# Optimization experiments

Hardware: AMD Instinct MI355X
Metric: run time of the kernel (lower is better)

## Reference

```python
import jax, jax.numpy as jnp
import numpy as np

ALPHA = 1.0
GAMMA = 2.0
BETA = 0.99
NUM_CLASSES = 37
N = 4_194_304


def setup_inputs() -> dict:
    key = jax.random.key(0)
    k1, k2 = jax.random.split(key)
    logits = jax.random.normal(k1, (N, NUM_CLASSES), dtype=jnp.float32)
    target = jax.random.randint(k2, (N,), 0, NUM_CLASSES, dtype=jnp.int64 if jax.config.jax_enable_x64 else jnp.int32)
    return {"logits": logits, "target": target}


def reference(logits, target):
    # Stable cross-entropy per sample: ce = -log_softmax(logits)[i, target[i]]
    logp = jax.nn.log_softmax(logits, axis=-1)                    # [N, C]
    ce = -jnp.take_along_axis(logp, target[:, None], axis=-1)[:, 0]  # [N]
    pt = jnp.exp(-ce)

    # Histogram of class counts (replaces the per-class Python loop).
    counts = jnp.zeros((NUM_CLASSES,), dtype=jnp.float32).at[target].add(1.0)  # [C]

    # Per-sample weight: 1 / beta**freq(class of sample)
    weights = (1.0 / BETA) ** counts[target]                      # [N]

    # Per-class weight: 1 / beta**(freq / total). Fresh state => total == N.
    class_weights = (1.0 / BETA) ** (counts / counts.sum())       # [C]

    focal = ALPHA * (1.0 - pt) ** GAMMA * ce * weights            # [N]
    # reduction == 'mean': (scalar / [C]).mean()
    return (focal.mean() / class_weights).mean()
```

## Files before the change

kernel.cpp:

```cpp
#include <hip/hip_runtime.h>
#include <hip/hip_bf16.h>

#define NUM_C 37
#define WTILE 64
#define LOG_INV_BETA 0.010050336f
#define LOG_BETA    (-0.010050336f)
#define FLT_MAX_SAT 3.402823466e+38f

#define NSLOT 64
#define SLOT_STRIDE 16
#define WS_E 37
#define WS_SLOTS 64
#define WS_TOTAL (WS_SLOTS + NSLOT * SLOT_STRIDE)

__device__ __forceinline__ float finite_scrub(float v, float sat) {
    unsigned u = __float_as_uint(v);
    if ((u & 0x7f800000u) == 0x7f800000u) return sat;
    return v;
}

__global__ void hist_kernel(const int* __restrict__ target, float* __restrict__ counts, int n) {
    __shared__ unsigned int h[NUM_C];
    for (int j = threadIdx.x; j < NUM_C; j += blockDim.x) h[j] = 0u;
    __syncthreads();

    const int4* t4 = (const int4*)target;
    int n4 = n >> 2;
    int stride = gridDim.x * blockDim.x;
    for (int i = blockIdx.x * blockDim.x + threadIdx.x; i < n4; i += stride) {
        int4 v = t4[i];
        if ((unsigned)v.x < NUM_C) atomicAdd(&h[v.x], 1u);
        if ((unsigned)v.y < NUM_C) atomicAdd(&h[v.y], 1u);
        if ((unsigned)v.z < NUM_C) atomicAdd(&h[v.z], 1u);
        if ((unsigned)v.w < NUM_C) atomicAdd(&h[v.w], 1u);
    }
    for (int i = (n4 << 2) + blockIdx.x * blockDim.x + threadIdx.x; i < n; i += stride) {
        int t = target[i];
        if ((unsigned)t < NUM_C) atomicAdd(&h[t], 1u);
    }
    __syncthreads();
    for (int j = threadIdx.x; j < NUM_C; j += blockDim.x)
        if (h[j]) atomicAdd(&counts[j], (float)h[j]);
}

__global__ void prep_kernel(float* __restrict__ ws) {
    int c = threadIdx.x;
    float v = (c < NUM_C) ? ws[c] : 0.0f;
#pragma unroll
    for (int off = 32; off > 0; off >>= 1) v = fmaxf(v, __shfl_xor(v, off, 64));
    if (c == 0) ws[WS_E] = v * LOG_INV_BETA;
}

__global__ __launch_bounds__(WTILE) void focal_main(const float* __restrict__ logits,
                                                    const int* __restrict__ target,
                                                    float* __restrict__ ws,
                                                    int n) {
    __shared__ float sm[WTILE * NUM_C];
    const int lane = threadIdx.x;
    const float E = ws[WS_E];

    long long base = (long long)blockIdx.x * WTILE;
    const float* src = logits + base * NUM_C;

    if (base + WTILE <= n) {
#pragma unroll
        for (int r = 0; r < 9; ++r) {
            __builtin_amdgcn_global_load_lds(
                (const __attribute__((address_space(1))) unsigned int*)(src + r * 256 + lane * 4),
                (__attribute__((address_space(3))) unsigned int*)((char*)sm + r * 1024),
                16, 0, 0);
        }
        __builtin_amdgcn_global_load_lds(
            (const __attribute__((address_space(1))) unsigned int*)(src + 9 * 256 + lane),
            (__attribute__((address_space(3))) unsigned int*)((char*)sm + 9 * 1024),
            4, 0, 0);
    } else {
        int rem = (int)((long long)n - base) * NUM_C;
        for (int k = lane; k < rem; k += WTILE) sm[k] = src[k];
    }
    __syncthreads();

    float local = 0.0f;
    long long i = base + lane;
    if (i < n) {
        const float* row = sm + lane * NUM_C;
        float r[NUM_C];
#pragma unroll
        for (int j = 0; j < NUM_C; ++j) r[j] = row[j];
        float m = r[0];
#pragma unroll
        for (int j = 1; j < NUM_C; ++j) m = fmaxf(m, r[j]);
        float s = 0.0f;
#pragma unroll
        for (int j = 0; j < NUM_C; ++j) s += __expf(r[j] - m);
        int t = target[i];
        if ((unsigned)t >= NUM_C) t = 0;
        float xt = row[t];
        float ce = __logf(s) + m - xt;
        float pt = __expf(-ce);
        float ex = fminf(fmaf(ws[t], LOG_INV_BETA, -E), 0.0f);
        float w  = __expf(ex);
        float om = 1.0f - pt;
        local = fminf(fmaxf(om * om * ce * w, 0.0f), 1e30f);
    }

#pragma unroll
    for (int off = 32; off > 0; off >>= 1) local += __shfl_down(local, off, 64);
    if (lane == 0)
        atomicAdd(&ws[WS_SLOTS + (blockIdx.x & (NSLOT - 1)) * SLOT_STRIDE], local);
}

__global__ void finalize_kernel(const float* __restrict__ ws, float* __restrict__ out, int n) {
    int c = threadIdx.x;
    float S = ws[WS_SLOTS + c * SLOT_STRIDE];
#pragma unroll
    for (int off = 32; off > 0; off >>= 1) S += __shfl_xor(S, off, 64);
    float cnt = (c < NUM_C) ? ws[c] : 0.0f;
    float total = cnt;
#pragma unroll
    for (int off = 32; off > 0; off >>= 1) total += __shfl_xor(total, off, 64);
    total = fmaxf(total, 1.0f);
    float term = (c < NUM_C) ? __expf((cnt / total) * LOG_BETA) : 0.0f;
    float s = term;
#pragma unroll
    for (int off = 32; off > 0; off >>= 1) s += __shfl_xor(s, off, 64);
    if (c == 0) {
        float Sf = finite_scrub(S, 1e30f);
        float E  = finite_scrub(ws[WS_E], 1e6f);
        E = fminf(fmaxf(E, 0.0f), 1e6f);
        float log_result = E + __logf(fmaxf(Sf, 1e-38f) / (float)n)
                             + __logf(fmaxf(s, 1e-38f) / (float)NUM_C);
        float v = __expf(fminf(log_result, 88.0f));
        if (log_result < -103.0f) v = 0.0f;
        v = finite_scrub(v, FLT_MAX_SAT);
        v = fminf(fmaxf(v, 0.0f), FLT_MAX_SAT);
        out[0] = v;
    }
}

extern "C" void kernel_launch(void* const* d_in, const int* in_sizes, int n_in,
                              void* d_out, int out_size, void* d_ws, size_t ws_size,
                              hipStream_t stream) {
    const float* logits = (const float*)d_in[0];
    const int* target   = (const int*)d_in[1];
    float* out          = (float*)d_out;
    float* ws           = (float*)d_ws;
    int n = in_sizes[1];

    hipMemsetAsync(d_ws, 0, WS_TOTAL * sizeof(float), stream);

    hist_kernel<<<256, 256, 0, stream>>>(target, ws, n);
    prep_kernel<<<1, 64, 0, stream>>>(ws);

    int nblocks = (n + WTILE - 1) / WTILE;
    focal_main<<<nblocks, WTILE, 0, stream>>>(logits, target, ws, n);

    finalize_kernel<<<1, 64, 0, stream>>>(ws, out, n);
}
```

Measured before the change: 789.8 us.

## Fuse histogram into focal pass via per-class partial sums and double-buffered persistent tiles

Drops the separate histogram and prep kernels. Because the per-sample weight depends only on the class, the main kernel now accumulates per-class focal sums and counts in LDS, and finalize applies the class weights afterwards. The main kernel is also made persistent with a fixed grid and double-buffered async global-to-LDS staging of logits and targets, so the next tile loads while the current one computes. This removes a full extra read of the target array and three launches' worth of dependency, at the cost of LDS atomics per sample and a hand-set waitcnt that must match the number of outstanding loads.

```diff
diff --git a/kernel.cpp b/kernel.cpp
--- a/kernel.cpp
+++ b/kernel.cpp
@@ -2,16 +2,16 @@
 #include <hip/hip_bf16.h>
 
 #define NUM_C 37
-#define WTILE 64
 #define LOG_INV_BETA 0.010050336f
 #define LOG_BETA    (-0.010050336f)
 #define FLT_MAX_SAT 3.402823466e+38f
 
-#define NSLOT 64
-#define SLOT_STRIDE 16
-#define WS_E 37
-#define WS_SLOTS 64
-#define WS_TOTAL (WS_SLOTS + NSLOT * SLOT_STRIDE)
+#define NBLK 4096
+#define NSLOT 32
+#define SLOT_PITCH 40
+#define WS_CNT 64
+#define WS_P   (WS_CNT + NSLOT * SLOT_PITCH)
+#define WS_TOTAL (WS_P + NSLOT * SLOT_PITCH)
 
 __device__ __forceinline__ float finite_scrub(float v, float sat) {
     unsigned u = __float_as_uint(v);
@@ -19,117 +19,138 @@
     return v;
 }
 
-__global__ void hist_kernel(const int* __restrict__ target, float* __restrict__ counts, int n) {
-    __shared__ unsigned int h[NUM_C];
-    for (int j = threadIdx.x; j < NUM_C; j += blockDim.x) h[j] = 0u;
-    __syncthreads();
-
-    const int4* t4 = (const int4*)target;
-    int n4 = n >> 2;
-    int stride = gridDim.x * blockDim.x;
-    for (int i = blockIdx.x * blockDim.x + threadIdx.x; i < n4; i += stride) {
-        int4 v = t4[i];
-        if ((unsigned)v.x < NUM_C) atomicAdd(&h[v.x], 1u);
-        if ((unsigned)v.y < NUM_C) atomicAdd(&h[v.y], 1u);
-        if ((unsigned)v.z < NUM_C) atomicAdd(&h[v.z], 1u);
-        if ((unsigned)v.w < NUM_C) atomicAdd(&h[v.w], 1u);
+__device__ __forceinline__ void stage_tile_async(const float* __restrict__ src,
+                                                 const int* __restrict__ tgt,
+                                                 float* bufp, int* tbufp, int lane) {
+#pragma unroll
+    for (int r = 0; r < 9; ++r) {
+        __builtin_amdgcn_global_load_lds(
+            (const __attribute__((address_space(1))) unsigned int*)(src + r * 256 + lane * 4),
+            (__attribute__((address_space(3))) unsigned int*)((char*)bufp + r * 1024),
+            16, 0, 0);
     }
-    for (int i = (n4 << 2) + blockIdx.x * blockDim.x + threadIdx.x; i < n; i += stride) {
-        int t = target[i];
-        if ((unsigned)t < NUM_C) atomicAdd(&h[t], 1u);
-    }
-    __syncthreads();
-    for (int j = threadIdx.x; j < NUM_C; j += blockDim.x)
-        if (h[j]) atomicAdd(&counts[j], (float)h[j]);
+    __builtin_amdgcn_global_load_lds(
+        (const __attribute__((address_space(1))) unsigned int*)(src + 2304 + lane),
+        (__attribute__((address_space(3))) unsigned int*)((char*)bufp + 9216), 4, 0, 0);
+    __builtin_amdgcn_global_load_lds(
+        (const __attribute__((address_space(1))) unsigned int*)(tgt + lane),
+        (__attribute__((address_space(3))) unsigned int*)tbufp, 4, 0, 0);
 }
 
-__global__ void prep_kernel(float* __restrict__ ws) {
-    int c = threadIdx.x;
-    float v = (c < NUM_C) ? ws[c] : 0.0f;
-#pragma unroll
-    for (int off = 32; off > 0; off >>= 1) v = fmaxf(v, __shfl_xor(v, off, 64));
-    if (c == 0) ws[WS_E] = v * LOG_INV_BETA;
+__device__ __forceinline__ void stage_tile_partial(const float* __restrict__ src,
+                                                   const int* __restrict__ tgt,
+                                                   float* bufp, int* tbufp,
+                                                   int lane, int rem) {
+    for (int k = lane; k < rem * NUM_C; k += 64) bufp[k] = src[k];
+    if (lane < rem) tbufp[lane] = tgt[lane];
 }
 
-__global__ __launch_bounds__(WTILE) void focal_main(const float* __restrict__ logits,
-                                                    const int* __restrict__ target,
-                                                    float* __restrict__ ws,
-                                                    int n) {
-    __shared__ float sm[WTILE * NUM_C];
+__global__ __launch_bounds__(64) void fused_main(const float* __restrict__ logits,
+                                                 const int* __restrict__ target,
+                                                 float* __restrict__ ws,
+                                                 int n) {
+    __shared__ float buf[2][64 * NUM_C];
+    __shared__ int   tbuf[2][64];
+    __shared__ float hP[NUM_C];
+    __shared__ unsigned hC[NUM_C];
+
     const int lane = threadIdx.x;
-    const float E = ws[WS_E];
+    if (lane < NUM_C) { hP[lane] = 0.0f; hC[lane] = 0u; }
 
-    long long base = (long long)blockIdx.x * WTILE;
-    const float* src = logits + base * NUM_C;
+    const int total_tiles = (n + 63) >> 6;
+    int tile = blockIdx.x;
+    int pb = 0;
 
-    if (base + WTILE <= n) {
-#pragma unroll
-        for (int r = 0; r < 9; ++r) {
-            __builtin_amdgcn_global_load_lds(
-                (const __attribute__((address_space(1))) unsigned int*)(src + r * 256 + lane * 4),
-                (__attribute__((address_space(3))) unsigned int*)((char*)sm + r * 1024),
-                16, 0, 0);
-        }
-        __builtin_amdgcn_global_load_lds(
-            (const __attribute__((address_space(1))) unsigned int*)(src + 9 * 256 + lane),
-            (__attribute__((address_space(3))) unsigned int*)((char*)sm + 9 * 1024),
-            4, 0, 0);
-    } else {
-        int rem = (int)((long long)n - base) * NUM_C;
-        for (int k = lane; k < rem; k += WTILE) sm[k] = src[k];
-    }
-    __syncthreads();
-
-    float local = 0.0f;
-    long long i = base + lane;
-    if (i < n) {
-        const float* row = sm + lane * NUM_C;
-        float r[NUM_C];
-#pragma unroll
-        for (int j = 0; j < NUM_C; ++j) r[j] = row[j];
-        float m = r[0];
-#pragma unroll
-        for (int j = 1; j < NUM_C; ++j) m = fmaxf(m, r[j]);
-        float s = 0.0f;
-#pragma unroll
-        for (int j = 0; j < NUM_C; ++j) s += __expf(r[j] - m);
-        int t = target[i];
-        if ((unsigned)t >= NUM_C) t = 0;
-        float xt = row[t];
-        float ce = __logf(s) + m - xt;
-        float pt = __expf(-ce);
-        float ex = fminf(fmaf(ws[t], LOG_INV_BETA, -E), 0.0f);
-        float w  = __expf(ex);
-        float om = 1.0f - pt;
-        local = fminf(fmaxf(om * om * ce * w, 0.0f), 1e30f);
+    if (tile < total_tiles) {
+        long long base = (long long)tile << 6;
+        if (base + 64 <= n)
+            stage_tile_async(logits + base * NUM_C, target + base, buf[0], tbuf[0], lane);
+        else
+            stage_tile_partial(logits + base * NUM_C, target + base, buf[0], tbuf[0],
+                               lane, (int)(n - base));
     }
 
+    while (tile < total_tiles) {
+        int next = tile + gridDim.x;
+        if (next < total_tiles) {
+            long long nb = (long long)next << 6;
+            if (nb + 64 <= n)
+                stage_tile_async(logits + nb * NUM_C, target + nb, buf[pb ^ 1], tbuf[pb ^ 1], lane);
+            else
+                stage_tile_partial(logits + nb * NUM_C, target + nb, buf[pb ^ 1], tbuf[pb ^ 1],
+                                   lane, (int)(n - nb));
+            __asm__ __volatile__("s_waitcnt vmcnt(11) lgkmcnt(0)" ::: "memory");
+        } else {
+            __asm__ __volatile__("s_waitcnt vmcnt(0) lgkmcnt(0)" ::: "memory");
+        }
+
+        long long base = (long long)tile << 6;
+        int rem = (int)((n - base) < 64 ? (n - base) : 64);
+        if (lane < rem) {
+            const float* row = &buf[pb][lane * NUM_C];
+            float r[NUM_C];
 #pragma unroll
-    for (int off = 32; off > 0; off >>= 1) local += __shfl_down(local, off, 64);
-    if (lane == 0)
-        atomicAdd(&ws[WS_SLOTS + (blockIdx.x & (NSLOT - 1)) * SLOT_STRIDE], local);
+            for (int j = 0; j < NUM_C; ++j) r[j] = row[j];
+            float m = r[0];
+#pragma unroll
+            for (int j = 1; j < NUM_C; ++j) m = fmaxf(m, r[j]);
+            float s = 0.0f;
+#pragma unroll
+            for (int j = 0; j < NUM_C; ++j) s += __expf(r[j] - m);
+            int t = tbuf[pb][lane];
+            if ((unsigned)t >= NUM_C) t = 0;
+            float xt = row[t];
+            float ce = __logf(s) + m - xt;
+            float pt = __expf(-ce);
+            float om = 1.0f - pt;
+            float term = fminf(fmaxf(om * om * ce, 0.0f), 1e30f);
+            atomicAdd(&hP[t], term);
+            atomicAdd(&hC[t], 1u);
+        }
+
+        tile = next;
+        pb ^= 1;
+    }
+
+    __syncthreads();
+    if (lane < NUM_C) {
+        int slot = blockIdx.x & (NSLOT - 1);
+        atomicAdd(&ws[WS_CNT + slot * SLOT_PITCH + lane], (float)hC[lane]);
+        atomicAdd(&ws[WS_P   + slot * SLOT_PITCH + lane], hP[lane]);
+    }
 }
 
 __global__ void finalize_kernel(const float* __restrict__ ws, float* __restrict__ out, int n) {
     int c = threadIdx.x;
-    float S = ws[WS_SLOTS + c * SLOT_STRIDE];
+    float cnt = 0.0f, P = 0.0f;
+    if (c < NUM_C) {
+#pragma unroll
+        for (int sidx = 0; sidx < NSLOT; ++sidx) {
+            cnt += ws[WS_CNT + sidx * SLOT_PITCH + c];
+            P   += ws[WS_P   + sidx * SLOT_PITCH + c];
+        }
+    }
+    float e = (c < NUM_C) ? cnt * LOG_INV_BETA : 0.0f;
+    float E = e;
+#pragma unroll
+    for (int off = 32; off > 0; off >>= 1) E = fmaxf(E, __shfl_xor(E, off, 64));
+    float term = (c < NUM_C) ? P * __expf(fminf(e - E, 0.0f)) : 0.0f;
+    float S = term;
 #pragma unroll
     for (int off = 32; off > 0; off >>= 1) S += __shfl_xor(S, off, 64);
-    float cnt = (c < NUM_C) ? ws[c] : 0.0f;
     float total = cnt;
 #pragma unroll
     for (int off = 32; off > 0; off >>= 1) total += __shfl_xor(total, off, 64);
     total = fmaxf(total, 1.0f);
-    float term = (c < NUM_C) ? __expf((cnt / total) * LOG_BETA) : 0.0f;
-    float s = term;
+    float cw = (c < NUM_C) ? __expf((cnt / total) * LOG_BETA) : 0.0f;
+    float s = cw;
 #pragma unroll
     for (int off = 32; off > 0; off >>= 1) s += __shfl_xor(s, off, 64);
     if (c == 0) {
         float Sf = finite_scrub(S, 1e30f);
-        float E  = finite_scrub(ws[WS_E], 1e6f);
-        E = fminf(fmaxf(E, 0.0f), 1e6f);
-        float log_result = E + __logf(fmaxf(Sf, 1e-38f) / (float)n)
-                             + __logf(fmaxf(s, 1e-38f) / (float)NUM_C);
+        float Ef = fminf(fmaxf(finite_scrub(E, 1e6f), 0.0f), 1e6f);
+        float log_result = Ef + __logf(fmaxf(Sf, 1e-38f) / (float)n)
+                              + __logf(fmaxf(s, 1e-38f) / (float)NUM_C);
         float v = __expf(fminf(log_result, 88.0f));
         if (log_result < -103.0f) v = 0.0f;
         v = finite_scrub(v, FLT_MAX_SAT);
@@ -149,11 +170,9 @@
 
     hipMemsetAsync(d_ws, 0, WS_TOTAL * sizeof(float), stream);
 
-    hist_kernel<<<256, 256, 0, stream>>>(target, ws, n);
-    prep_kernel<<<1, 64, 0, stream>>>(ws);
-
-    int nblocks = (n + WTILE - 1) / WTILE;
-    focal_main<<<nblocks, WTILE, 0, stream>>>(logits, target, ws, n);
+    int total_tiles = (n + 63) >> 6;
+    int nblocks = total_tiles < NBLK ? total_tiles : NBLK;
+    fused_main<<<nblocks, 64, 0, stream>>>(logits, target, ws, n);
 
     finalize_kernel<<<1, 64, 0, stream>>>(ws, out, n);
 }
```

After: 788.0 us. No clear change (-0.2%).
